# Kernel optimization log

Hardware: AMD Instinct MI355X
Metric: run time of the kernel (lower is better)

The kernel has to match this reference:

```python
import jax, jax.numpy as jnp
import numpy as np

N = 4096
IN_DIM = 256
OUT_DIM = 256
E = 131072


def setup_inputs() -> dict:
    key = jax.random.key(0)
    ks = jax.random.split(key, 8)
    x = jax.random.normal(ks[0], (N, IN_DIM), dtype=jnp.float32)
    edge_index = jax.random.randint(ks[1], (2, E), 0, N, dtype=jnp.int64)
    lap = jax.random.normal(ks[2], (N, N), dtype=jnp.float32)
    d_inv = jax.random.normal(ks[3], (N, N), dtype=jnp.float32)
    # parameters
    W_high = jax.random.normal(ks[4], (IN_DIM, OUT_DIM), dtype=jnp.float32) / np.sqrt(IN_DIM)
    W_conv = jax.random.normal(ks[5], (IN_DIM, OUT_DIM), dtype=jnp.float32) / np.sqrt(IN_DIM)
    b_conv = jnp.zeros((OUT_DIM,), dtype=jnp.float32)
    aL = jax.random.uniform(ks[6], (1,), dtype=jnp.float32)
    aH = jax.random.uniform(ks[7], (1,), dtype=jnp.float32)
    return {"x": x, "edge_index": edge_index, "lap": lap, "d_inv": d_inv,
            "W_high": W_high, "W_conv": W_conv, "b_conv": b_conv,
            "aL": aL, "aH": aH}


def _gcn_conv(x, edge_index, W, b, num_nodes):
    # PyG GCNConv: add self-loops, symmetric normalization, aggregate at target.
    src, dst = edge_index[0], edge_index[1]
    loop = jnp.arange(num_nodes, dtype=edge_index.dtype)
    src_f = jnp.concatenate([src, loop])
    dst_f = jnp.concatenate([dst, loop])
    deg = jax.ops.segment_sum(jnp.ones_like(dst_f, dtype=x.dtype), dst_f,
                              num_segments=num_nodes)
    deg_inv_sqrt = jnp.where(deg > 0, jax.lax.rsqrt(jnp.maximum(deg, 1e-12)), 0.0)
    norm = deg_inv_sqrt[src_f] * deg_inv_sqrt[dst_f]  # [E+N]
    xw = x @ W                                        # [N, out]
    msgs = xw[src_f] * norm[:, None]                  # [E+N, out]
    out = jax.ops.segment_sum(msgs, dst_f, num_segments=num_nodes)
    return out + b


def reference(x, edge_index, lap, d_inv, W_high, W_conv, b_conv, aL, aH):
    # high-pass branch: Lhp = d_inv @ lap @ d_inv; Hh = Lhp @ relu(x @ W_high)
    Lhp = (d_inv @ lap) @ d_inv
    Hh = Lhp @ jax.nn.relu(x @ W_high)
    # low-pass branch: GCNConv
    Hl = _gcn_conv(x, edge_index, W_conv, b_conv, x.shape[0])
    return aL * Hl + aH * Hh
```

## Files before the change

kernel.cpp:

```cpp
#include <hip/hip_runtime.h>

#define NN 4096
#define DD 256
#define EE 131072

typedef __attribute__((ext_vector_type(8))) short s16x8;
typedef __attribute__((ext_vector_type(4))) float f32x4;

__device__ __forceinline__ unsigned short f2bf(float f) {
  unsigned u = __builtin_bit_cast(unsigned, f);
  u += 0x7FFFu + ((u >> 16) & 1u);
  return (unsigned short)(u >> 16);
}

__device__ __forceinline__ ushort4 cvt4(f32x4 v) {
  ushort4 r;
  r.x = f2bf(v[0]); r.y = f2bf(v[1]); r.z = f2bf(v[2]); r.w = f2bf(v[3]);
  return r;
}

__device__ __forceinline__ unsigned cvt2_rhu(float a, float b) {
  unsigned ua = __builtin_bit_cast(unsigned, a) + 0x8000u;
  unsigned ub = __builtin_bit_cast(unsigned, b) + 0x8000u;
  return __builtin_amdgcn_perm(ub, ua, 0x07060302u);
}

__device__ __forceinline__ uint4 pack8(f32x4 a, f32x4 b) {
  uint4 r;
  r.x = cvt2_rhu(a[0], a[1]); r.y = cvt2_rhu(a[2], a[3]);
  r.z = cvt2_rhu(b[0], b[1]); r.w = cvt2_rhu(b[2], b[3]);
  return r;
}


__global__ void k_prep(const int* __restrict__ ei, int* __restrict__ deg,
                       const float* __restrict__ Wh, const float* __restrict__ Wc,
                       unsigned short* __restrict__ WFh, unsigned short* __restrict__ WFc) {
  int t = blockIdx.x * 256 + threadIdx.x;
  if (t < EE) {
    atomicAdd(&deg[ei[EE + t]], 1);
  } else {
    int idx = t - EE;
    int which = idx >> 16;
    int r = idx & 65535;
    int n = r & 255, k = r >> 8;
    const float* W = which ? Wc : Wh;
    unsigned short* WF = which ? WFc : WFh;
    long fidx = ((long)((n >> 4) * 8 + (k >> 5))) * 512 +
                (((k >> 3) & 3) * 16 + (n & 15)) * 8 + (k & 7);
    WF[fidx] = f2bf(W[k * 256 + n]);
  }
}

__global__ void k_scan(const int* __restrict__ deg, int* __restrict__ row_start,
                       float* __restrict__ dis) {
  __shared__ int part[1024];
  int t = threadIdx.x;
  int d0 = deg[4 * t + 0], d1 = deg[4 * t + 1], d2 = deg[4 * t + 2], d3 = deg[4 * t + 3];
  int s = d0 + d1 + d2 + d3;
  part[t] = s;
  __syncthreads();
  for (int off = 1; off < 1024; off <<= 1) {
    int add = (t >= off) ? part[t - off] : 0;
    __syncthreads();
    part[t] += add;
    __syncthreads();
  }
  int base = part[t] - s;
  row_start[4 * t + 0] = base;
  row_start[4 * t + 1] = base + d0;
  row_start[4 * t + 2] = base + d0 + d1;
  row_start[4 * t + 3] = base + d0 + d1 + d2;
  if (t == 1023) row_start[4096] = part[t];
  dis[4 * t + 0] = rsqrtf((float)d0 + 1.0f);
  dis[4 * t + 1] = rsqrtf((float)d1 + 1.0f);
  dis[4 * t + 2] = rsqrtf((float)d2 + 1.0f);
  dis[4 * t + 3] = rsqrtf((float)d3 + 1.0f);
}

__global__ void k_scatter(const int* __restrict__ ei, const int* __restrict__ row_start,
                          int* __restrict__ cursor, int* __restrict__ csr) {
  int e = blockIdx.x * 256 + threadIdx.x;
  if (e < EE) {
    int s = ei[e];
    int d = ei[EE + e];
    int p = atomicAdd(&cursor[d], 1);
    csr[row_start[d] + p] = s;
  }
}

__global__ __launch_bounds__(512) void k_xw(const float* __restrict__ x,
                                            const unsigned short* __restrict__ WFh,
                                            const unsigned short* __restrict__ WFc,
                                            unsigned short* __restrict__ RF,
                                            float* __restrict__ XWs,
                                            const float* __restrict__ dis) {
  __shared__ alignas(16) unsigned short Abuf[16][264];
  const int tid = threadIdx.x;
  const int w = tid >> 6, lane = tid & 63;
  const int quad = lane >> 4, l16 = lane & 15, quad8 = quad * 8;
  const int m0 = blockIdx.x * 16;

  {
    int srow = tid >> 5, scolf = (tid & 31) * 8;
    const float* ap = x + (long)(m0 + srow) * DD + scolf;
    f32x4 a0 = *(const f32x4*)ap;
    f32x4 a1 = *(const f32x4*)(ap + 4);
    *(uint4*)&Abuf[srow][scolf] = pack8(a0, a1);
  }
  __syncthreads();

  const bool hi = (w < 4);
  const int wo = hi ? w : (w - 4);
  const unsigned short* WF = hi ? WFh : WFc;
  const unsigned short* bp = WF + lane * 8;

  f32x4 acc[4] = {{0,0,0,0},{0,0,0,0},{0,0,0,0},{0,0,0,0}};
#pragma unroll
  for (int q = 0; q < 8; ++q) {
    s16x8 af = *(const s16x8*)&Abuf[l16][q * 32 + quad8];
#pragma unroll
    for (int s = 0; s < 4; ++s) {
      s16x8 bf = *(const s16x8*)(bp + ((long)((4 * wo + s) * 8 + q)) * 512);
      acc[s] = __builtin_amdgcn_mfma_f32_16x16x32_bf16(af, bf, acc[s], 0, 0, 0);
    }
  }

  if (hi) {
    const int kc = m0 >> 5;
    const int qp = ((m0 >> 4) & 1) * 2 + (quad >> 1);
    const int j0 = (quad & 1) * 4;
#pragma unroll
    for (int s = 0; s < 4; ++s) {
      int t = 4 * wo + s;
      f32x4 v = acc[s];
      f32x4 z;
      z[0] = v[0] > 0.f ? v[0] : 0.f;
      z[1] = v[1] > 0.f ? v[1] : 0.f;
      z[2] = v[2] > 0.f ? v[2] : 0.f;
      z[3] = v[3] > 0.f ? v[3] : 0.f;
      long idx = ((long)(t * 128 + kc)) * 512 + (qp * 16 + l16) * 8 + j0;
      *(ushort4*)(RF + idx) = cvt4(z);
    }
  } else {
    float dm[4];
#pragma unroll
    for (int r = 0; r < 4; ++r) dm[r] = dis[m0 + quad * 4 + r];
#pragma unroll
    for (int s = 0; s < 4; ++s) {
      int col = 64 * wo + 16 * s + l16;
#pragma unroll
      for (int r = 0; r < 4; ++r)
        XWs[(long)(m0 + quad * 4 + r) * DD + col] = dm[r] * acc[s][r];
    }
  }
}

__global__ void k_agg(const float* __restrict__ XWs, const int* __restrict__ row_start,
                      const int* __restrict__ csr, const float* __restrict__ dis,
                      float* __restrict__ Hl) {
  const int i = blockIdx.x;
  const int t = threadIdx.x;
  const int b0 = row_start[i], b1 = row_start[i + 1];
  float acc = XWs[(long)i * DD + t];
  int j = b0;
  for (; j + 4 <= b1; j += 4) {
    int s0 = csr[j], s1 = csr[j + 1], s2 = csr[j + 2], s3 = csr[j + 3];
    float v0 = XWs[(long)s0 * DD + t];
    float v1 = XWs[(long)s1 * DD + t];
    float v2 = XWs[(long)s2 * DD + t];
    float v3 = XWs[(long)s3 * DD + t];
    acc += (v0 + v1) + (v2 + v3);
  }
  for (; j < b1; ++j) acc += XWs[(long)csr[j] * DD + t];
  Hl[(long)i * DD + t] = dis[i] * acc;
}

template <int EPI>
__global__ __launch_bounds__(512) void k_mm2(const float* __restrict__ A,
                                             const unsigned short* __restrict__ BF,
                                             unsigned short* __restrict__ CF,
                                             float* __restrict__ outF,
                                             const float* __restrict__ Hl,
                                             const float* __restrict__ bconv,
                                             const float* __restrict__ aLp,
                                             const float* __restrict__ aHp) {
  __shared__ alignas(16) unsigned short Abuf[2][32][264];
  const int tid = threadIdx.x;
  const int w = tid >> 6, lane = tid & 63;
  const int quad = lane >> 4, l16 = lane & 15, quad8 = quad * 8;
  const int tile = blockIdx.x & 127, half = blockIdx.x >> 7;
  const int m0 = tile * 32;
  const int tglob = half * 8 + w;

  const int arow = tid >> 4;
  const int acolf = (tid & 15) * 16;
  const float* aptr = A + (long)(m0 + arow) * NN + acolf;

  {
    f32x4 c0 = *(const f32x4*)(aptr + 0);
    f32x4 c1 = *(const f32x4*)(aptr + 4);
    f32x4 c2 = *(const f32x4*)(aptr + 8);
    f32x4 c3 = *(const f32x4*)(aptr + 12);
    *(uint4*)&Abuf[0][arow][acolf] = pack8(c0, c1);
    *(uint4*)&Abuf[0][arow][acolf + 8] = pack8(c2, c3);
  }
  f32x4 anext[4];
#pragma unroll
  for (int i = 0; i < 4; ++i) anext[i] = *(const f32x4*)(aptr + 256 + 4 * i);
  __syncthreads();

  f32x4 acc[2] = {{0,0,0,0},{0,0,0,0}};
  const unsigned short* bbase = BF + ((long)tglob * 128) * 512 + lane * 8;

  for (int s = 0; s < 16; ++s) {
    const int cur = s & 1;
    f32x4 afut[4];
    if (s + 2 < 16) {
#pragma unroll
      for (int i = 0; i < 4; ++i)
        afut[i] = *(const f32x4*)(aptr + (s + 2) * 256 + 4 * i);
    } else {
#pragma unroll
      for (int i = 0; i < 4; ++i) afut[i] = anext[i];
    }

    const unsigned short* bs = bbase + ((long)s * 8) * 512;
#pragma unroll
    for (int c8 = 0; c8 < 8; ++c8) {
      s16x8 bf = *(const s16x8*)(bs + c8 * 512);
      s16x8 a0 = *(const s16x8*)&Abuf[cur][l16][c8 * 32 + quad8];
      s16x8 a1 = *(const s16x8*)&Abuf[cur][16 + l16][c8 * 32 + quad8];
      acc[0] = __builtin_amdgcn_mfma_f32_16x16x32_bf16(a0, bf, acc[0], 0, 0, 0);
      acc[1] = __builtin_amdgcn_mfma_f32_16x16x32_bf16(a1, bf, acc[1], 0, 0, 0);
    }

    if (s + 1 < 16) {
      *(uint4*)&Abuf[1 - cur][arow][acolf] = pack8(anext[0], anext[1]);
      *(uint4*)&Abuf[1 - cur][arow][acolf + 8] = pack8(anext[2], anext[3]);
    }
    __syncthreads();
#pragma unroll
    for (int i = 0; i < 4; ++i) anext[i] = afut[i];
  }

  if constexpr (EPI == 0) {
    const int kc = m0 >> 5;
#pragma unroll
    for (int mu = 0; mu < 2; ++mu) {
      int qp = mu * 2 + (quad >> 1);
      int j0 = (quad & 1) * 4;
      long idx = ((long)(tglob * 128 + kc)) * 512 + (qp * 16 + l16) * 8 + j0;
      *(ushort4*)(CF + idx) = cvt4(acc[mu]);
    }
  } else {
    __shared__ float obuf[32][132];
#pragma unroll
    for (int mu = 0; mu < 2; ++mu)
#pragma unroll
      for (int r = 0; r < 4; ++r)
        obuf[mu * 16 + quad * 4 + r][w * 16 + l16] = acc[mu][r];
    __syncthreads();
    const float aLv = aLp[0], aHv = aHp[0];
    const int orow = tid >> 4;
    const int ocol = (tid & 15) * 8;
    const int gcol = half * 128 + ocol;
#pragma unroll
    for (int j = 0; j < 2; ++j) {
      f32x4 cc = *(const f32x4*)&obuf[orow][ocol + 4 * j];
      f32x4 h = *(const f32x4*)(Hl + (long)(m0 + orow) * DD + gcol + 4 * j);
      f32x4 bc = *(const f32x4*)(bconv + gcol + 4 * j);
      f32x4 res;
      res[0] = aHv * cc[0] + aLv * (h[0] + bc[0]);
      res[1] = aHv * cc[1] + aLv * (h[1] + bc[1]);
      res[2] = aHv * cc[2] + aLv * (h[2] + bc[2]);
      res[3] = aHv * cc[3] + aLv * (h[3] + bc[3]);
      *(f32x4*)(outF + (long)(m0 + orow) * DD + gcol + 4 * j) = res;
    }
  }
}

extern "C" void kernel_launch(void* const* d_in, const int* in_sizes, int n_in,
                              void* d_out, int out_size, void* d_ws, size_t ws_size,
                              hipStream_t stream) {
  const float* x     = (const float*)d_in[0];
  const int*   ei    = (const int*)d_in[1];
  const float* lap   = (const float*)d_in[2];
  const float* dinv  = (const float*)d_in[3];
  const float* Wh    = (const float*)d_in[4];
  const float* Wc    = (const float*)d_in[5];
  const float* bconv = (const float*)d_in[6];
  const float* aL    = (const float*)d_in[7];
  const float* aH    = (const float*)d_in[8];
  float* out = (float*)d_out;
  char* ws = (char*)d_ws;

  int* deg        = (int*)(ws);
  int* cursor     = (int*)(ws + (16 << 10));
  int* row_start  = (int*)(ws + (32 << 10));
  int* csr        = (int*)(ws + (64 << 10));
  float* dis      = (float*)(ws + (576 << 10));
  unsigned short* WFh = (unsigned short*)(ws + (1l << 20));
  unsigned short* WFc = (unsigned short*)(ws + (1l << 20) + (128 << 10));
  unsigned short* RF  = (unsigned short*)(ws + (2l << 20));
  unsigned short* T1F = (unsigned short*)(ws + (4l << 20));
  unsigned short* T2F = (unsigned short*)(ws + (6l << 20));
  float* XWs = (float*)(ws + (8l << 20));
  float* Hl  = (float*)(ws + (12l << 20));

  hipMemsetAsync(ws, 0, 32 << 10, stream);

  k_prep<<<1024, 256, 0, stream>>>(ei, deg, Wh, Wc, WFh, WFc);
  k_scan<<<1, 1024, 0, stream>>>(deg, row_start, dis);
  k_scatter<<<512, 256, 0, stream>>>(ei, row_start, cursor, csr);
  k_xw<<<256, 512, 0, stream>>>(x, WFh, WFc, RF, XWs, dis);
  k_agg<<<4096, 256, 0, stream>>>(XWs, row_start, csr, dis, Hl);

  k_mm2<0><<<256, 512, 0, stream>>>(dinv, RF, T1F, nullptr, nullptr, nullptr, nullptr, nullptr);
  k_mm2<0><<<256, 512, 0, stream>>>(lap, T1F, T2F, nullptr, nullptr, nullptr, nullptr, nullptr);
  k_mm2<3><<<256, 512, 0, stream>>>(dinv, T2F, nullptr, out, Hl, bconv, aL, aH);
}
```

Before: 273.9 us.

## Restructure skinny GEMM into 4-wave blocks with register-prefetched B and 512 blocks

The three N×N by N×256 GEMMs now run in 256-thread blocks, each covering 32 rows by 64 output columns, with 512 blocks instead of 256. B fragments are double-buffered in registers and prefetched one K-step ahead, and each thread loads two A rows per step. The aggregation kernel is unrolled to eight neighbor loads per iteration to keep more gathers in flight. More blocks raise occupancy and B-prefetch hides load latency, but the fp32 A matrix is now read by four column-quarter blocks instead of two, doubling A traffic through L2.

```diff
diff --git a/kernel.cpp b/kernel.cpp
--- a/kernel.cpp
+++ b/kernel.cpp
@@ -164,20 +164,55 @@
   const int b0 = row_start[i], b1 = row_start[i + 1];
   float acc = XWs[(long)i * DD + t];
   int j = b0;
-  for (; j + 4 <= b1; j += 4) {
+  for (; j + 8 <= b1; j += 8) {
     int s0 = csr[j], s1 = csr[j + 1], s2 = csr[j + 2], s3 = csr[j + 3];
+    int s4 = csr[j + 4], s5 = csr[j + 5], s6 = csr[j + 6], s7 = csr[j + 7];
     float v0 = XWs[(long)s0 * DD + t];
     float v1 = XWs[(long)s1 * DD + t];
     float v2 = XWs[(long)s2 * DD + t];
     float v3 = XWs[(long)s3 * DD + t];
-    acc += (v0 + v1) + (v2 + v3);
+    float v4 = XWs[(long)s4 * DD + t];
+    float v5 = XWs[(long)s5 * DD + t];
+    float v6 = XWs[(long)s6 * DD + t];
+    float v7 = XWs[(long)s7 * DD + t];
+    acc += ((v0 + v1) + (v2 + v3)) + ((v4 + v5) + (v6 + v7));
   }
   for (; j < b1; ++j) acc += XWs[(long)csr[j] * DD + t];
   Hl[(long)i * DD + t] = dis[i] * acc;
 }
 
+#define MM3_STEP(sv, BCUR, BNXT, CUR, NXT)                                        \
+  {                                                                               \
+    const int sn = (sv) + 1;                                                      \
+    f32x4 an[8];                                                                  \
+    if (sn < 16) {                                                                \
+      _Pragma("unroll")                                                           \
+      for (int i = 0; i < 4; ++i) {                                               \
+        an[i] = *(const f32x4*)(aptr0 + sn * 256 + 4 * i);                        \
+        an[4 + i] = *(const f32x4*)(aptr1 + sn * 256 + 4 * i);                    \
+      }                                                                           \
+      _Pragma("unroll")                                                           \
+      for (int c8 = 0; c8 < 8; ++c8)                                              \
+        BNXT[c8] = *(const s16x8*)(bbase + ((long)(sn * 8 + c8)) * 512);          \
+    }                                                                             \
+    _Pragma("unroll")                                                             \
+    for (int c8 = 0; c8 < 8; ++c8) {                                              \
+      s16x8 a0 = *(const s16x8*)&Abuf[CUR][l16][c8 * 32 + quad8];                 \
+      s16x8 a1 = *(const s16x8*)&Abuf[CUR][16 + l16][c8 * 32 + quad8];            \
+      acc[0] = __builtin_amdgcn_mfma_f32_16x16x32_bf16(a0, BCUR[c8], acc[0], 0, 0, 0); \
+      acc[1] = __builtin_amdgcn_mfma_f32_16x16x32_bf16(a1, BCUR[c8], acc[1], 0, 0, 0); \
+    }                                                                             \
+    if (sn < 16) {                                                                \
+      *(uint4*)&Abuf[NXT][arow][acolf] = pack8(an[0], an[1]);                     \
+      *(uint4*)&Abuf[NXT][arow][acolf + 8] = pack8(an[2], an[3]);                 \
+      *(uint4*)&Abuf[NXT][arow + 16][acolf] = pack8(an[4], an[5]);                \
+      *(uint4*)&Abuf[NXT][arow + 16][acolf + 8] = pack8(an[6], an[7]);            \
+    }                                                                             \
+    __syncthreads();                                                              \
+  }
+
 template <int EPI>
-__global__ __launch_bounds__(512) void k_mm2(const float* __restrict__ A,
+__global__ __launch_bounds__(256) void k_mm3(const float* __restrict__ A,
                                              const unsigned short* __restrict__ BF,
                                              unsigned short* __restrict__ CF,
                                              float* __restrict__ outF,
@@ -189,72 +224,54 @@
   const int tid = threadIdx.x;
   const int w = tid >> 6, lane = tid & 63;
   const int quad = lane >> 4, l16 = lane & 15, quad8 = quad * 8;
-  const int tile = blockIdx.x & 127, half = blockIdx.x >> 7;
-  const int m0 = tile * 32;
-  const int tglob = half * 8 + w;
+  const int m = blockIdx.x & 127;
+  const int q = blockIdx.x >> 7;
+  const int m0 = m * 32;
+  const int tglob = q * 4 + w;
 
   const int arow = tid >> 4;
   const int acolf = (tid & 15) * 16;
-  const float* aptr = A + (long)(m0 + arow) * NN + acolf;
+  const float* aptr0 = A + (long)(m0 + arow) * NN + acolf;
+  const float* aptr1 = aptr0 + (long)16 * NN;
+
+  const unsigned short* bbase = BF + ((long)tglob * 128) * 512 + lane * 8;
+
+  f32x4 acc[2] = {{0,0,0,0},{0,0,0,0}};
+  s16x8 bbA[8], bbB[8];
 
   {
-    f32x4 c0 = *(const f32x4*)(aptr + 0);
-    f32x4 c1 = *(const f32x4*)(aptr + 4);
-    f32x4 c2 = *(const f32x4*)(aptr + 8);
-    f32x4 c3 = *(const f32x4*)(aptr + 12);
-    *(uint4*)&Abuf[0][arow][acolf] = pack8(c0, c1);
-    *(uint4*)&Abuf[0][arow][acolf + 8] = pack8(c2, c3);
-  }
-  f32x4 anext[4];
-#pragma unroll
-  for (int i = 0; i < 4; ++i) anext[i] = *(const f32x4*)(aptr + 256 + 4 * i);
+    f32x4 r0 = *(const f32x4*)(aptr0 + 0);
+    f32x4 r1 = *(const f32x4*)(aptr0 + 4);
+    f32x4 r2 = *(const f32x4*)(aptr0 + 8);
+    f32x4 r3 = *(const f32x4*)(aptr0 + 12);
+    f32x4 r4 = *(const f32x4*)(aptr1 + 0);
+    f32x4 r5 = *(const f32x4*)(aptr1 + 4);
+    f32x4 r6 = *(const f32x4*)(aptr1 + 8);
+    f32x4 r7 = *(const f32x4*)(aptr1 + 12);
+    *(uint4*)&Abuf[0][arow][acolf] = pack8(r0, r1);
+    *(uint4*)&Abuf[0][arow][acolf + 8] = pack8(r2, r3);
+    *(uint4*)&Abuf[0][arow + 16][acolf] = pack8(r4, r5);
+    *(uint4*)&Abuf[0][arow + 16][acolf + 8] = pack8(r6, r7);
+  }
+#pragma unroll
+  for (int c8 = 0; c8 < 8; ++c8) bbA[c8] = *(const s16x8*)(bbase + c8 * 512);
   __syncthreads();
 
-  f32x4 acc[2] = {{0,0,0,0},{0,0,0,0}};
-  const unsigned short* bbase = BF + ((long)tglob * 128) * 512 + lane * 8;
-
-  for (int s = 0; s < 16; ++s) {
-    const int cur = s & 1;
-    f32x4 afut[4];
-    if (s + 2 < 16) {
-#pragma unroll
-      for (int i = 0; i < 4; ++i)
-        afut[i] = *(const f32x4*)(aptr + (s + 2) * 256 + 4 * i);
-    } else {
-#pragma unroll
-      for (int i = 0; i < 4; ++i) afut[i] = anext[i];
-    }
-
-    const unsigned short* bs = bbase + ((long)s * 8) * 512;
-#pragma unroll
-    for (int c8 = 0; c8 < 8; ++c8) {
-      s16x8 bf = *(const s16x8*)(bs + c8 * 512);
-      s16x8 a0 = *(const s16x8*)&Abuf[cur][l16][c8 * 32 + quad8];
-      s16x8 a1 = *(const s16x8*)&Abuf[cur][16 + l16][c8 * 32 + quad8];
-      acc[0] = __builtin_amdgcn_mfma_f32_16x16x32_bf16(a0, bf, acc[0], 0, 0, 0);
-      acc[1] = __builtin_amdgcn_mfma_f32_16x16x32_bf16(a1, bf, acc[1], 0, 0, 0);
-    }
-
-    if (s + 1 < 16) {
-      *(uint4*)&Abuf[1 - cur][arow][acolf] = pack8(anext[0], anext[1]);
-      *(uint4*)&Abuf[1 - cur][arow][acolf + 8] = pack8(anext[2], anext[3]);
-    }
-    __syncthreads();
-#pragma unroll
-    for (int i = 0; i < 4; ++i) anext[i] = afut[i];
+  for (int ss = 0; ss < 8; ++ss) {
+    MM3_STEP(2 * ss, bbA, bbB, 0, 1)
+    MM3_STEP(2 * ss + 1, bbB, bbA, 1, 0)
   }
 
   if constexpr (EPI == 0) {
-    const int kc = m0 >> 5;
 #pragma unroll
     for (int mu = 0; mu < 2; ++mu) {
       int qp = mu * 2 + (quad >> 1);
       int j0 = (quad & 1) * 4;
-      long idx = ((long)(tglob * 128 + kc)) * 512 + (qp * 16 + l16) * 8 + j0;
+      long idx = ((long)(tglob * 128 + m)) * 512 + (qp * 16 + l16) * 8 + j0;
       *(ushort4*)(CF + idx) = cvt4(acc[mu]);
     }
   } else {
-    __shared__ float obuf[32][132];
+    __shared__ float obuf[32][68];
 #pragma unroll
     for (int mu = 0; mu < 2; ++mu)
 #pragma unroll
@@ -262,9 +279,9 @@
         obuf[mu * 16 + quad * 4 + r][w * 16 + l16] = acc[mu][r];
     __syncthreads();
     const float aLv = aLp[0], aHv = aHp[0];
-    const int orow = tid >> 4;
-    const int ocol = (tid & 15) * 8;
-    const int gcol = half * 128 + ocol;
+    const int orow = tid >> 3;
+    const int ocol = (tid & 7) * 8;
+    const int gcol = q * 64 + ocol;
 #pragma unroll
     for (int j = 0; j < 2; ++j) {
       f32x4 cc = *(const f32x4*)&obuf[orow][ocol + 4 * j];
@@ -316,7 +333,7 @@
   k_xw<<<256, 512, 0, stream>>>(x, WFh, WFc, RF, XWs, dis);
   k_agg<<<4096, 256, 0, stream>>>(XWs, row_start, csr, dis, Hl);
 
-  k_mm2<0><<<256, 512, 0, stream>>>(dinv, RF, T1F, nullptr, nullptr, nullptr, nullptr, nullptr);
-  k_mm2<0><<<256, 512, 0, stream>>>(lap, T1F, T2F, nullptr, nullptr, nullptr, nullptr, nullptr);
-  k_mm2<3><<<256, 512, 0, stream>>>(dinv, T2F, nullptr, out, Hl, bconv, aL, aH);
-}
+  k_mm3<0><<<512, 256, 0, stream>>>(dinv, RF, T1F, nullptr, nullptr, nullptr, nullptr, nullptr);
+  k_mm3<0><<<512, 256, 0, stream>>>(lap, T1F, T2F, nullptr, nullptr, nullptr, nullptr, nullptr);
+  k_mm3<3><<<512, 256, 0, stream>>>(dinv, T2F, nullptr, out, Hl, bconv, aL, aH);
+}
```

Result: slower. 286.2 us (+4.5%).
